# Kernel tuning notes

Measured on AMD Instinct MI355X. Metric: run time of the kernel, lower is better.

## Reference

```python
import jax, jax.numpy as jnp
import numpy as np
import math

B, T, E, K, V = 64, 512, 512, 512, 512


def setup_inputs() -> dict:
    key = jax.random.key(0)
    ks = jax.random.split(key, 7)
    s = 1.0 / math.sqrt(E)
    return {
        "x": jax.random.normal(ks[0], (B, T, E), dtype=jnp.float32),
        "Wq": jax.random.normal(ks[1], (E, K), dtype=jnp.float32) * s,
        "bq": jnp.zeros((K,), dtype=jnp.float32),
        "Wk": jax.random.normal(ks[2], (E, K), dtype=jnp.float32) * s,
        "bk": jnp.zeros((K,), dtype=jnp.float32),
        "Wv": jax.random.normal(ks[3], (E, V), dtype=jnp.float32) * s,
        "bv": jnp.zeros((V,), dtype=jnp.float32),
    }


def reference(x, Wq, bq, Wk, bk, Wv, bv):
    # Linear projections (N, T, E) -> (N, T, K/V)
    q = x @ Wq + bq
    k = x @ Wk + bk
    v = x @ Wv + bv
    # weight_pos_graph(query, keys) interpreted as Q K^T: (N, T, T)
    scores = jnp.einsum("btd,bsd->bts", q, k)
    # mask[j, i] = 1 if i > j  -> strict upper triangle masked to -inf (causal)
    mask = jnp.triu(jnp.ones((T, T), dtype=bool), k=1)
    scores = jnp.where(mask, -jnp.inf, scores)
    # NOTE: original softmaxes over dim=1 (the query/row axis), not dim=-1
    attn = jax.nn.softmax(scores / math.sqrt(K), axis=1)
    # bmm(attn, values): (N, T, T) @ (N, T, V) -> (N, T, V)
    return jnp.einsum("bts,bsv->btv", attn, v)
```

## Files before the change

### kernel.cpp

```cpp
#include <hip/hip_runtime.h>
#include <hip/hip_bf16.h>
#include <math.h>

#define B_DIM 64
#define T_DIM 512
#define E_DIM 512

typedef __bf16 bf16_t;
typedef bf16_t bf16x8 __attribute__((ext_vector_type(8)));
typedef float  f32x4  __attribute__((ext_vector_type(4)));

typedef unsigned char __attribute__((address_space(1))) uc_g;
typedef unsigned char __attribute__((address_space(3))) uc_l;

__device__ __forceinline__ void gl_lds16(const void* g, void* l) {
  __builtin_amdgcn_global_load_lds((const uc_g*)g, (uc_l*)l, 16, 0, 0);
}

__global__ __launch_bounds__(256) void cvtx_kernel(const float* __restrict__ x,
                                                   bf16_t* __restrict__ xb) {
  const size_t t = (size_t)blockIdx.x * 256 + threadIdx.x;
  const float4 a = ((const float4*)x)[t * 2];
  const float4 b = ((const float4*)x)[t * 2 + 1];
  bf16x8 o;
  o[0] = (bf16_t)a.x; o[1] = (bf16_t)a.y; o[2] = (bf16_t)a.z; o[3] = (bf16_t)a.w;
  o[4] = (bf16_t)b.x; o[5] = (bf16_t)b.y; o[6] = (bf16_t)b.z; o[7] = (bf16_t)b.w;
  *(bf16x8*)(xb + t * 8) = o;
}

__global__ __launch_bounds__(256) void wtr_kernel(const float* __restrict__ W0,
                                                  const float* __restrict__ W1,
                                                  const float* __restrict__ W2,
                                                  bf16_t* __restrict__ WTall) {
  const int z = blockIdx.z;
  const float* W = z == 0 ? W0 : (z == 1 ? W1 : W2);
  bf16_t* O = WTall + (size_t)z * 512 * E_DIM;
  __shared__ float tile[32][33];
  const int tx = threadIdx.x, ty = threadIdx.y;
  const int r0 = blockIdx.y * 32, c0 = blockIdx.x * 32;
#pragma unroll
  for (int i = 0; i < 4; ++i)
    tile[ty + i * 8][tx] = W[(size_t)(r0 + ty + i * 8) * E_DIM + c0 + tx];
  __syncthreads();
#pragma unroll
  for (int i = 0; i < 4; ++i)
    O[(size_t)(c0 + ty + i * 8) * E_DIM + r0 + tx] = (bf16_t)tile[tx][ty + i * 8];
}

__global__ __launch_bounds__(256) void bcat_kernel(const float* __restrict__ b0,
                                                   const float* __restrict__ b1,
                                                   const float* __restrict__ b2,
                                                   float* __restrict__ bb) {
  const int i = blockIdx.x * 256 + threadIdx.x;
  bb[i] = i < 512 ? b0[i] : (i < 1024 ? b1[i - 512] : b2[i - 1024]);
}

__global__ __launch_bounds__(256) void zero_kernel(float4* __restrict__ p) {
  p[blockIdx.x * 256 + threadIdx.x] = make_float4(0.f, 0.f, 0.f, 0.f);
}

__global__ __launch_bounds__(512) void vtr_kernel(const bf16_t* __restrict__ Vb,
                                                  const float* __restrict__ Dsum,
                                                  bf16_t* __restrict__ VT, int ldv) {
  const int b = blockIdx.z;
  __shared__ bf16_t tile[64][65];
  const int tx = threadIdx.x, ty = threadIdx.y;
  const bf16_t* src = Vb + (size_t)b * T_DIM * ldv;
  const float* Ds = Dsum + (size_t)b * T_DIM;
  bf16_t* dst = VT + (size_t)b * T_DIM * T_DIM;
  const int r0 = blockIdx.y * 64, c0 = blockIdx.x * 64;
#pragma unroll
  for (int i = 0; i < 8; ++i) {
    const int s = r0 + ty + i * 8;
    const float inv = 1.0f / Ds[s];
    tile[ty + i * 8][tx] = (bf16_t)((float)src[(size_t)s * ldv + c0 + tx] * inv);
  }
  __syncthreads();
#pragma unroll
  for (int i = 0; i < 8; ++i)
    dst[(size_t)(c0 + ty + i * 8) * T_DIM + r0 + tx] = tile[tx][ty + i * 8];
}

template <int EPI>
__global__ __launch_bounds__(256)
void gemm_nt(const bf16_t* __restrict__ A, const bf16_t* __restrict__ Bt,
             void* __restrict__ Cv, const float* __restrict__ bias,
             float* __restrict__ Dsum,
             int K, int lda, int ldb, int ldc,
             long sA, long sB, long sC, float scale) {
  __shared__ bf16_t lA[128 * 64];
  __shared__ bf16_t lB[128 * 64];
  const int bz = blockIdx.z;
  const int bm = blockIdx.x, bn = blockIdx.y;
  if (EPI == 1 && bn > bm) return;

  const int tid = threadIdx.x;
  const int wid = tid >> 6, lane = tid & 63;
  const int wr = wid >> 1, wc = wid & 1;
  const int l15 = lane & 15, lk = lane >> 4;

  const long crow0 = (long)bm * 128 + wr * 64 + lk * 4;
  const int ccol0 = bn * 128 + wc * 64 + l15;

  const bf16_t* Ab = A + (long)bz * sA;
  const bf16_t* Bb = Bt + (long)bz * sB;

  f32x4 acc[4][4] = {};

  const int srow = tid >> 3;
  const int scol = (tid & 7) * 8;
  const bf16_t* gA = Ab + (long)(bm * 128 + srow) * lda + scol;
  const bf16_t* gB = Bb + (long)(bn * 128 + srow) * ldb + scol;
  const int lbase = wid * 512;

  const int Kend = (EPI == 2) ? (bm + 1) * 128 : K;

  for (int k0 = 0; k0 < Kend; k0 += 64) {
#pragma unroll
    for (int c = 0; c < 4; ++c) {
      gl_lds16(gA + (long)(c * 32) * lda + k0, lA + c * 2048 + lbase);
      gl_lds16(gB + (long)(c * 32) * ldb + k0, lB + c * 2048 + lbase);
    }
    __syncthreads();
#pragma unroll
    for (int ks = 0; ks < 2; ++ks) {
      bf16x8 af[4], bfr[4];
#pragma unroll
      for (int m = 0; m < 4; ++m)
        af[m] = *(const bf16x8*)&lA[(wr * 64 + m * 16 + l15) * 64 + ks * 32 + lk * 8];
#pragma unroll
      for (int n = 0; n < 4; ++n)
        bfr[n] = *(const bf16x8*)&lB[(wc * 64 + n * 16 + l15) * 64 + ks * 32 + lk * 8];
#pragma unroll
      for (int m = 0; m < 4; ++m)
#pragma unroll
        for (int n = 0; n < 4; ++n)
          acc[m][n] = __builtin_amdgcn_mfma_f32_16x16x32_bf16(af[m], bfr[n], acc[m][n], 0, 0, 0);
    }
    __syncthreads();
  }

  if constexpr (EPI == 0) {
    bf16_t* C = (bf16_t*)Cv + (long)bz * sC;
#pragma unroll
    for (int m = 0; m < 4; ++m)
#pragma unroll
      for (int n = 0; n < 4; ++n) {
        const int col = ccol0 + n * 16;
        const float bv = bias[col];
#pragma unroll
        for (int r = 0; r < 4; ++r)
          C[(crow0 + m * 16 + r) * (long)ldc + col] = (bf16_t)(acc[m][n][r] + bv);
      }
  } else if constexpr (EPI == 1) {
    bf16_t* C = (bf16_t*)Cv + (long)bz * sC;
    float ts[4] = {0.f, 0.f, 0.f, 0.f};
#pragma unroll
    for (int m = 0; m < 4; ++m)
#pragma unroll
      for (int n = 0; n < 4; ++n) {
        const int col = ccol0 + n * 16;
#pragma unroll
        for (int r = 0; r < 4; ++r) {
          const long row = crow0 + m * 16 + r;
          float e = 0.f;
          if (col <= row) e = __expf(acc[m][n][r] * scale);
          const bf16_t eb = (bf16_t)e;
          C[row * (long)ldc + col] = eb;
          ts[n] += (float)eb;
        }
      }
#pragma unroll
    for (int n = 0; n < 4; ++n) {
      ts[n] += __shfl_xor(ts[n], 16);
      ts[n] += __shfl_xor(ts[n], 32);
    }
    float* colsum = (float*)lA;
    if (tid < 128) colsum[tid] = 0.f;
    __syncthreads();
    if (lk == 0) {
#pragma unroll
      for (int n = 0; n < 4; ++n)
        atomicAdd(&colsum[wc * 64 + n * 16 + l15], ts[n]);
    }
    __syncthreads();
    if (tid < 128)
      atomicAdd(&Dsum[(long)bz * T_DIM + bn * 128 + tid], colsum[tid]);
  } else {
    float* C = (float*)Cv + (long)bz * sC;
#pragma unroll
    for (int m = 0; m < 4; ++m)
#pragma unroll
      for (int n = 0; n < 4; ++n) {
        const int col = ccol0 + n * 16;
#pragma unroll
        for (int r = 0; r < 4; ++r)
          C[(crow0 + m * 16 + r) * (long)ldc + col] = acc[m][n][r];
      }
  }
}

extern "C" void kernel_launch(void* const* d_in, const int* in_sizes, int n_in,
                              void* d_out, int out_size, void* d_ws, size_t ws_size,
                              hipStream_t stream) {
  const float* x  = (const float*)d_in[0];
  const float* Wq = (const float*)d_in[1];
  const float* bq = (const float*)d_in[2];
  const float* Wk = (const float*)d_in[3];
  const float* bk = (const float*)d_in[4];
  const float* Wv = (const float*)d_in[5];
  const float* bv = (const float*)d_in[6];
  float* out = (float*)d_out;

  char* ws = (char*)d_ws;
  const size_t SZ = (size_t)B_DIM * T_DIM * E_DIM * 2;
  bf16_t* xb    = (bf16_t*)(ws);
  bf16_t* P     = (bf16_t*)(ws);
  bf16_t* qkv   = (bf16_t*)(ws + SZ);
  bf16_t* vT    = (bf16_t*)(ws + SZ + 3 * SZ);
  bf16_t* WTall = (bf16_t*)(ws + 5 * SZ);
  float*  bcat  = (float*)(ws + 5 * SZ + 1572864);
  float*  Dsum  = (float*)(ws + 5 * SZ + 1572864 + 8192);

  const int M = B_DIM * T_DIM;
  const long sQKV = (long)T_DIM * 1536;
  const long bstr = (long)T_DIM * T_DIM;
  const float scale = 1.0f / sqrtf((float)E_DIM);

  cvtx_kernel<<<dim3(8192), dim3(256), 0, stream>>>(x, xb);
  wtr_kernel<<<dim3(16, 16, 3), dim3(32, 8), 0, stream>>>(Wq, Wk, Wv, WTall);
  bcat_kernel<<<dim3(6), dim3(256), 0, stream>>>(bq, bk, bv, bcat);
  gemm_nt<0><<<dim3(256, 12, 1), dim3(256), 0, stream>>>(
      xb, WTall, qkv, bcat, nullptr, 512, 512, 512, 1536, 0, 0, 0, 0.f);
  zero_kernel<<<dim3(32), dim3(256), 0, stream>>>((float4*)Dsum);
  gemm_nt<1><<<dim3(4, 4, B_DIM), dim3(256), 0, stream>>>(
      qkv, qkv + 512, P, nullptr, Dsum, 512, 1536, 1536, T_DIM,
      sQKV, sQKV, bstr, scale);
  vtr_kernel<<<dim3(8, 8, B_DIM), dim3(64, 8), 0, stream>>>(qkv + 1024, Dsum, vT, 1536);
  gemm_nt<2><<<dim3(4, 4, B_DIM), dim3(256), 0, stream>>>(
      P, vT, out, nullptr, nullptr, 512, T_DIM, T_DIM, T_DIM,
      bstr, bstr, bstr, 1.f);
}
```

Baseline: 304.6 us.

## Replace QKV projection GEMM with 256x256-tile triple-buffered 512-thread kernel

Adds a dedicated QKV projection kernel that uses 256x256 output tiles with 8 waves, a three-stage LDS ring filled by direct global-to-LDS loads, XOR-swizzled LDS addressing, and a block-index remap for L2 locality. Loads for stage k+2 are issued while MFMAs on stage k run, with explicit waitcnt/barriers and setprio to favour the matrix ops. The aim is more data reuse per tile and better overlap of memory and compute in the largest GEMM. It costs a higher register count (128 accumulators per thread) and hand-written synchronisation that is easy to get wrong.

```diff
diff --git a/kernel.cpp b/kernel.cpp
--- a/kernel.cpp
+++ b/kernel.cpp
@@ -79,6 +79,98 @@
 #pragma unroll
   for (int i = 0; i < 8; ++i)
     dst[(size_t)(c0 + ty + i * 8) * T_DIM + r0 + tx] = tile[tx][ty + i * 8];
+}
+
+__global__ __launch_bounds__(512)
+void gemm256_qkv(const bf16_t* __restrict__ A, const bf16_t* __restrict__ Bt,
+                 bf16_t* __restrict__ C, const float* __restrict__ bias) {
+  __shared__ bf16_t lds[3][2][8192];
+  const int tid = threadIdx.x;
+
+  int lin = blockIdx.y * 128 + blockIdx.x;
+  lin = (lin & 7) * 96 + (lin >> 3);
+  const int bm = lin & 127;
+  const int bn = lin >> 7;
+
+  const int w = tid >> 6, j = tid & 63;
+  const int srow = w * 16 + (j >> 2);
+  const int scol = ((j & 3) ^ ((j >> 3) & 3)) * 8;
+  const bf16_t* gA = A + (long)(bm * 256 + srow) * 512 + scol;
+  const bf16_t* gB = Bt + (long)(bn * 256 + srow) * 512 + scol;
+
+  const int l15 = tid & 15, lk = (tid >> 4) & 3;
+  const int kperm = (lk ^ ((l15 >> 1) & 3)) * 8;
+  const int wr = w >> 2, wc = w & 3;
+
+#define STG_A(kt, buf) { gl_lds16(gA + (long)(kt) * 32, &lds[buf][0][w * 512]); \
+                         gl_lds16(gA + (long)(kt) * 32 + 128 * 512, &lds[buf][0][4096 + w * 512]); }
+#define STG_B(kt, buf) { gl_lds16(gB + (long)(kt) * 32, &lds[buf][1][w * 512]); \
+                         gl_lds16(gB + (long)(kt) * 32 + 128 * 512, &lds[buf][1][4096 + w * 512]); }
+
+  f32x4 acc[8][4] = {};
+
+  STG_A(0, 0); STG_B(0, 0);
+  STG_A(1, 1); STG_B(1, 1);
+  asm volatile("s_waitcnt vmcnt(4)" ::: "memory");
+  asm volatile("s_barrier" ::: "memory");
+
+  int cb = 0;
+  for (int kt = 0; kt < 16; ++kt) {
+    const int sb = (cb == 0) ? 2 : cb - 1;
+    const bf16_t* lA_ = lds[cb][0];
+    const bf16_t* lB_ = lds[cb][1];
+
+    bf16x8 bfr[4], af0[4];
+#pragma unroll
+    for (int n = 0; n < 4; ++n)
+      bfr[n] = *(const bf16x8*)&lB_[(wc * 64 + n * 16 + l15) * 32 + kperm];
+#pragma unroll
+    for (int m = 0; m < 4; ++m)
+      af0[m] = *(const bf16x8*)&lA_[(wr * 128 + m * 16 + l15) * 32 + kperm];
+    if (kt < 14) STG_A(kt + 2, sb);
+    asm volatile("s_barrier" ::: "memory");
+    __builtin_amdgcn_s_setprio(1);
+#pragma unroll
+    for (int m = 0; m < 4; ++m)
+#pragma unroll
+      for (int n = 0; n < 4; ++n)
+        acc[m][n] = __builtin_amdgcn_mfma_f32_16x16x32_bf16(af0[m], bfr[n], acc[m][n], 0, 0, 0);
+    __builtin_amdgcn_s_setprio(0);
+    asm volatile("s_barrier" ::: "memory");
+
+    bf16x8 af1[4];
+#pragma unroll
+    for (int m = 0; m < 4; ++m)
+      af1[m] = *(const bf16x8*)&lA_[(wr * 128 + 64 + m * 16 + l15) * 32 + kperm];
+    if (kt < 14) STG_B(kt + 2, sb);
+    if (kt < 14)       asm volatile("s_waitcnt vmcnt(4)" ::: "memory");
+    else if (kt == 14) asm volatile("s_waitcnt vmcnt(0)" ::: "memory");
+    asm volatile("s_barrier" ::: "memory");
+    __builtin_amdgcn_s_setprio(1);
+#pragma unroll
+    for (int m = 0; m < 4; ++m)
+#pragma unroll
+      for (int n = 0; n < 4; ++n)
+        acc[4 + m][n] = __builtin_amdgcn_mfma_f32_16x16x32_bf16(af1[m], bfr[n], acc[4 + m][n], 0, 0, 0);
+    __builtin_amdgcn_s_setprio(0);
+    asm volatile("s_barrier" ::: "memory");
+    cb = (cb == 2) ? 0 : cb + 1;
+  }
+#undef STG_A
+#undef STG_B
+
+#pragma unroll
+  for (int mm = 0; mm < 8; ++mm) {
+    const long row0 = (long)bm * 256 + wr * 128 + mm * 16 + lk * 4;
+#pragma unroll
+    for (int n = 0; n < 4; ++n) {
+      const int col = bn * 256 + wc * 64 + n * 16 + l15;
+      const float bv = bias[col];
+#pragma unroll
+      for (int r = 0; r < 4; ++r)
+        C[(row0 + r) * 1536 + col] = (bf16_t)(acc[mm][n][r] + bv);
+    }
+  }
 }
 
 template <int EPI>
@@ -140,19 +232,7 @@
     __syncthreads();
   }
 
-  if constexpr (EPI == 0) {
-    bf16_t* C = (bf16_t*)Cv + (long)bz * sC;
-#pragma unroll
-    for (int m = 0; m < 4; ++m)
-#pragma unroll
-      for (int n = 0; n < 4; ++n) {
-        const int col = ccol0 + n * 16;
-        const float bv = bias[col];
-#pragma unroll
-        for (int r = 0; r < 4; ++r)
-          C[(crow0 + m * 16 + r) * (long)ldc + col] = (bf16_t)(acc[m][n][r] + bv);
-      }
-  } else if constexpr (EPI == 1) {
+  if constexpr (EPI == 1) {
     bf16_t* C = (bf16_t*)Cv + (long)bz * sC;
     float ts[4] = {0.f, 0.f, 0.f, 0.f};
 #pragma unroll
@@ -222,7 +302,6 @@
   float*  bcat  = (float*)(ws + 5 * SZ + 1572864);
   float*  Dsum  = (float*)(ws + 5 * SZ + 1572864 + 8192);
 
-  const int M = B_DIM * T_DIM;
   const long sQKV = (long)T_DIM * 1536;
   const long bstr = (long)T_DIM * T_DIM;
   const float scale = 1.0f / sqrtf((float)E_DIM);
@@ -230,8 +309,7 @@
   cvtx_kernel<<<dim3(8192), dim3(256), 0, stream>>>(x, xb);
   wtr_kernel<<<dim3(16, 16, 3), dim3(32, 8), 0, stream>>>(Wq, Wk, Wv, WTall);
   bcat_kernel<<<dim3(6), dim3(256), 0, stream>>>(bq, bk, bv, bcat);
-  gemm_nt<0><<<dim3(256, 12, 1), dim3(256), 0, stream>>>(
-      xb, WTall, qkv, bcat, nullptr, 512, 512, 512, 1536, 0, 0, 0, 0.f);
+  gemm256_qkv<<<dim3(128, 6), dim3(512), 0, stream>>>(xb, WTall, qkv, bcat);
   zero_kernel<<<dim3(32), dim3(256), 0, stream>>>((float4*)Dsum);
   gemm_nt<1><<<dim3(4, 4, B_DIM), dim3(256), 0, stream>>>(
       qkv, qkv + 512, P, nullptr, Dsum, 512, 1536, 1536, T_DIM,
```

Measured after the change: 282.7 us. 7.2% less time.

## Restructure GEMMs with triple-buffered LDS pipeline, 128x256 tiles, swizzle

Applied to the files above, without the earlier changes.

Replaces the single-buffered 128x128 GEMM with a 512-thread, 128x256-tile kernel that uses a three-stage LDS ring loaded via global_load_lds. Loads for step kt+2 are issued ahead with explicit vmcnt waits and raw barriers, and MFMA issue gets raised priority. LDS uses an XOR swizzle to avoid bank conflicts, and the projection GEMM gets a grouped block-index remap for L2 reuse. The aim is to hide global-load latency and cut per-tile overhead. The trade-offs are more LDS per block, lower occupancy, and coarser causal tile skipping in the score and PV GEMMs.

```diff
diff --git a/kernel.cpp b/kernel.cpp
--- a/kernel.cpp
+++ b/kernel.cpp
@@ -82,87 +82,113 @@
 }
 
 template <int EPI>
-__global__ __launch_bounds__(256)
-void gemm_nt(const bf16_t* __restrict__ A, const bf16_t* __restrict__ Bt,
-             void* __restrict__ Cv, const float* __restrict__ bias,
-             float* __restrict__ Dsum,
-             int K, int lda, int ldb, int ldc,
-             long sA, long sB, long sC, float scale) {
-  __shared__ bf16_t lA[128 * 64];
-  __shared__ bf16_t lB[128 * 64];
-  const int bz = blockIdx.z;
-  const int bm = blockIdx.x, bn = blockIdx.y;
-  if (EPI == 1 && bn > bm) return;
-
+__global__ __launch_bounds__(512)
+void gemm_p(const bf16_t* __restrict__ A, const bf16_t* __restrict__ Bt,
+            void* __restrict__ Cv, const float* __restrict__ bias,
+            float* __restrict__ Dsum,
+            int lda, int ldb, int ldc, long sA, long sB, long sC, float scale) {
+  __shared__ bf16_t lds[3][12288];
   const int tid = threadIdx.x;
-  const int wid = tid >> 6, lane = tid & 63;
-  const int wr = wid >> 1, wc = wid & 1;
-  const int l15 = lane & 15, lk = lane >> 4;
-
-  const long crow0 = (long)bm * 128 + wr * 64 + lk * 4;
-  const int ccol0 = bn * 128 + wc * 64 + l15;
-
-  const bf16_t* Ab = A + (long)bz * sA;
-  const bf16_t* Bb = Bt + (long)bz * sB;
+
+  int bm, bn, bz, NT;
+  if (EPI == 0) {
+    const int lin = blockIdx.x;
+    const int nl = (lin & 7) * 192 + (lin >> 3);
+    bm = nl / 6; bn = nl - bm * 6;
+    bz = 0; NT = 16;
+  } else {
+    bm = blockIdx.x; bn = blockIdx.y; bz = blockIdx.z;
+    if (EPI == 1 && 2 * bn > bm) return;
+    NT = (EPI == 2) ? (bm + 1) * 4 : 16;
+  }
+
+  const bf16_t* Ab = A + bz * sA + (long)bm * 128 * lda;
+  const bf16_t* Bb = Bt + bz * sB + (long)bn * 256 * ldb;
+
+  const int strow = tid >> 2, stg = tid & 3;
+  const int sgg = stg ^ ((strow >> 1) & 3);
+  const bf16_t* gA  = Ab + (long)strow * lda + sgg * 8;
+  const bf16_t* gB0 = Bb + (long)strow * ldb + sgg * 8;
+  const bf16_t* gB1 = gB0 + (long)128 * ldb;
+
+#define STAGE(kt, buf) { gl_lds16(gA  + (long)(kt) * 32, &lds[buf][tid * 8]);        \
+                         gl_lds16(gB0 + (long)(kt) * 32, &lds[buf][4096 + tid * 8]); \
+                         gl_lds16(gB1 + (long)(kt) * 32, &lds[buf][8192 + tid * 8]); }
+
+  const int l15 = tid & 15, lk = (tid >> 4) & 3;
+  const int w = tid >> 6, wr = w >> 2, wc = w & 3;
+  int aoff[4], boff[4];
+#pragma unroll
+  for (int m = 0; m < 4; ++m) {
+    const int row = wr * 64 + m * 16 + l15;
+    aoff[m] = row * 32 + (lk ^ ((row >> 1) & 3)) * 8;
+  }
+#pragma unroll
+  for (int n = 0; n < 4; ++n) {
+    const int row = wc * 64 + n * 16 + l15;
+    boff[n] = 4096 + row * 32 + (lk ^ ((row >> 1) & 3)) * 8;
+  }
 
   f32x4 acc[4][4] = {};
 
-  const int srow = tid >> 3;
-  const int scol = (tid & 7) * 8;
-  const bf16_t* gA = Ab + (long)(bm * 128 + srow) * lda + scol;
-  const bf16_t* gB = Bb + (long)(bn * 128 + srow) * ldb + scol;
-  const int lbase = wid * 512;
-
-  const int Kend = (EPI == 2) ? (bm + 1) * 128 : K;
-
-  for (int k0 = 0; k0 < Kend; k0 += 64) {
-#pragma unroll
-    for (int c = 0; c < 4; ++c) {
-      gl_lds16(gA + (long)(c * 32) * lda + k0, lA + c * 2048 + lbase);
-      gl_lds16(gB + (long)(c * 32) * ldb + k0, lB + c * 2048 + lbase);
-    }
-    __syncthreads();
-#pragma unroll
-    for (int ks = 0; ks < 2; ++ks) {
-      bf16x8 af[4], bfr[4];
-#pragma unroll
-      for (int m = 0; m < 4; ++m)
-        af[m] = *(const bf16x8*)&lA[(wr * 64 + m * 16 + l15) * 64 + ks * 32 + lk * 8];
+  STAGE(0, 0); STAGE(1, 1);
+  asm volatile("s_waitcnt vmcnt(3)" ::: "memory");
+  asm volatile("s_barrier" ::: "memory");
+
+  int cb = 0;
+  for (int kt = 0; kt < NT; ++kt) {
+    bf16x8 af[4], bfr[4];
+#pragma unroll
+    for (int m = 0; m < 4; ++m) af[m] = *(const bf16x8*)&lds[cb][aoff[m]];
+#pragma unroll
+    for (int n = 0; n < 4; ++n) bfr[n] = *(const bf16x8*)&lds[cb][boff[n]];
+    const int sb = (cb == 0) ? 2 : cb - 1;
+    if (kt + 2 < NT) {
+      STAGE(kt + 2, sb);
+      asm volatile("s_waitcnt vmcnt(3)" ::: "memory");
+    } else if (kt + 2 == NT) {
+      asm volatile("s_waitcnt vmcnt(0)" ::: "memory");
+    }
+    asm volatile("s_barrier" ::: "memory");
+    __builtin_amdgcn_s_setprio(1);
+#pragma unroll
+    for (int m = 0; m < 4; ++m)
 #pragma unroll
       for (int n = 0; n < 4; ++n)
-        bfr[n] = *(const bf16x8*)&lB[(wc * 64 + n * 16 + l15) * 64 + ks * 32 + lk * 8];
-#pragma unroll
-      for (int m = 0; m < 4; ++m)
-#pragma unroll
-        for (int n = 0; n < 4; ++n)
-          acc[m][n] = __builtin_amdgcn_mfma_f32_16x16x32_bf16(af[m], bfr[n], acc[m][n], 0, 0, 0);
-    }
-    __syncthreads();
-  }
+        acc[m][n] = __builtin_amdgcn_mfma_f32_16x16x32_bf16(af[m], bfr[n], acc[m][n], 0, 0, 0);
+    __builtin_amdgcn_s_setprio(0);
+    asm volatile("s_barrier" ::: "memory");
+    cb = (cb == 2) ? 0 : cb + 1;
+  }
+#undef STAGE
 
   if constexpr (EPI == 0) {
-    bf16_t* C = (bf16_t*)Cv + (long)bz * sC;
-#pragma unroll
-    for (int m = 0; m < 4; ++m)
+    bf16_t* C = (bf16_t*)Cv;
+#pragma unroll
+    for (int m = 0; m < 4; ++m) {
+      const long row0 = (long)bm * 128 + wr * 64 + m * 16 + lk * 4;
 #pragma unroll
       for (int n = 0; n < 4; ++n) {
-        const int col = ccol0 + n * 16;
+        const int col = bn * 256 + wc * 64 + n * 16 + l15;
         const float bv = bias[col];
 #pragma unroll
         for (int r = 0; r < 4; ++r)
-          C[(crow0 + m * 16 + r) * (long)ldc + col] = (bf16_t)(acc[m][n][r] + bv);
+          C[(row0 + r) * (long)ldc + col] = (bf16_t)(acc[m][n][r] + bv);
       }
+    }
   } else if constexpr (EPI == 1) {
-    bf16_t* C = (bf16_t*)Cv + (long)bz * sC;
+    bf16_t* C = (bf16_t*)Cv + bz * sC;
     float ts[4] = {0.f, 0.f, 0.f, 0.f};
 #pragma unroll
-    for (int m = 0; m < 4; ++m)
+    for (int m = 0; m < 4; ++m) {
+      const long row0 = (long)bm * 128 + wr * 64 + m * 16 + lk * 4;
 #pragma unroll
       for (int n = 0; n < 4; ++n) {
-        const int col = ccol0 + n * 16;
+        const int lcol = wc * 64 + n * 16 + l15;
+        const int col = bn * 256 + lcol;
 #pragma unroll
         for (int r = 0; r < 4; ++r) {
-          const long row = crow0 + m * 16 + r;
+          const long row = row0 + r;
           float e = 0.f;
           if (col <= row) e = __expf(acc[m][n][r] * scale);
           const bf16_t eb = (bf16_t)e;
@@ -170,13 +196,14 @@
           ts[n] += (float)eb;
         }
       }
+    }
 #pragma unroll
     for (int n = 0; n < 4; ++n) {
       ts[n] += __shfl_xor(ts[n], 16);
       ts[n] += __shfl_xor(ts[n], 32);
     }
-    float* colsum = (float*)lA;
-    if (tid < 128) colsum[tid] = 0.f;
+    float* colsum = (float*)&lds[0][0];
+    if (tid < 256) colsum[tid] = 0.f;
     __syncthreads();
     if (lk == 0) {
 #pragma unroll
@@ -184,19 +211,21 @@
         atomicAdd(&colsum[wc * 64 + n * 16 + l15], ts[n]);
     }
     __syncthreads();
-    if (tid < 128)
-      atomicAdd(&Dsum[(long)bz * T_DIM + bn * 128 + tid], colsum[tid]);
+    if (tid < 256)
+      atomicAdd(&Dsum[(long)bz * T_DIM + bn * 256 + tid], colsum[tid]);
   } else {
-    float* C = (float*)Cv + (long)bz * sC;
-#pragma unroll
-    for (int m = 0; m < 4; ++m)
+    float* C = (float*)Cv + bz * sC;
+#pragma unroll
+    for (int m = 0; m < 4; ++m) {
+      const long row0 = (long)bm * 128 + wr * 64 + m * 16 + lk * 4;
 #pragma unroll
       for (int n = 0; n < 4; ++n) {
-        const int col = ccol0 + n * 16;
+        const int col = bn * 256 + wc * 64 + n * 16 + l15;
 #pragma unroll
         for (int r = 0; r < 4; ++r)
-          C[(crow0 + m * 16 + r) * (long)ldc + col] = acc[m][n][r];
+          C[(row0 + r) * (long)ldc + col] = acc[m][n][r];
       }
+    }
   }
 }
 
@@ -222,7 +251,6 @@
   float*  bcat  = (float*)(ws + 5 * SZ + 1572864);
   float*  Dsum  = (float*)(ws + 5 * SZ + 1572864 + 8192);
 
-  const int M = B_DIM * T_DIM;
   const long sQKV = (long)T_DIM * 1536;
   const long bstr = (long)T_DIM * T_DIM;
   const float scale = 1.0f / sqrtf((float)E_DIM);
@@ -230,14 +258,12 @@
   cvtx_kernel<<<dim3(8192), dim3(256), 0, stream>>>(x, xb);
   wtr_kernel<<<dim3(16, 16, 3), dim3(32, 8), 0, stream>>>(Wq, Wk, Wv, WTall);
   bcat_kernel<<<dim3(6), dim3(256), 0, stream>>>(bq, bk, bv, bcat);
-  gemm_nt<0><<<dim3(256, 12, 1), dim3(256), 0, stream>>>(
-      xb, WTall, qkv, bcat, nullptr, 512, 512, 512, 1536, 0, 0, 0, 0.f);
+  gemm_p<0><<<dim3(1536), dim3(512), 0, stream>>>(
+      xb, WTall, qkv, bcat, nullptr, 512, 512, 1536, 0, 0, 0, 0.f);
   zero_kernel<<<dim3(32), dim3(256), 0, stream>>>((float4*)Dsum);
-  gemm_nt<1><<<dim3(4, 4, B_DIM), dim3(256), 0, stream>>>(
-      qkv, qkv + 512, P, nullptr, Dsum, 512, 1536, 1536, T_DIM,
-      sQKV, sQKV, bstr, scale);
+  gemm_p<1><<<dim3(4, 2, B_DIM), dim3(512), 0, stream>>>(
+      qkv, qkv + 512, P, nullptr, Dsum, 1536, 1536, T_DIM, sQKV, sQKV, bstr, scale);
   vtr_kernel<<<dim3(8, 8, B_DIM), dim3(64, 8), 0, stream>>>(qkv + 1024, Dsum, vT, 1536);
-  gemm_nt<2><<<dim3(4, 4, B_DIM), dim3(256), 0, stream>>>(
-      P, vT, out, nullptr, nullptr, 512, T_DIM, T_DIM, T_DIM,
-      bstr, bstr, bstr, 1.f);
-}
+  gemm_p<2><<<dim3(4, 2, B_DIM), dim3(512), 0, stream>>>(
+      P, vT, out, nullptr, nullptr, 512, 512, T_DIM, bstr, bstr, bstr, 1.f);
+}
```

Result: faster. 276.0 us (-9.4%).
